# Kernel tuning notes

Measured on AMD Instinct MI355X. Metric: run time of the kernel, lower is better.

Reference implementation:

```python
import jax, jax.numpy as jnp
import numpy as np

NUM_GRAPHS = 1024
HIDDEN = 256
N_NODES = 500000


def setup_inputs() -> dict:
    key = jax.random.key(0)
    k1, k2, k3, k4 = jax.random.split(key, 4)
    x = jax.random.normal(k1, (N_NODES, HIDDEN), dtype=jnp.float32)
    batch = jnp.sort(jax.random.randint(k2, (N_NODES,), 0, NUM_GRAPHS, dtype=jnp.int64))
    # attention = nn.Linear(hidden_dim, 1): weight [1, hidden], bias [1]
    bound = 1.0 / np.sqrt(HIDDEN)
    att_w = jax.random.uniform(k3, (HIDDEN, 1), dtype=jnp.float32, minval=-bound, maxval=bound)
    att_b = jax.random.uniform(k4, (1,), dtype=jnp.float32, minval=-bound, maxval=bound)
    return {"x": x, "batch": batch, "att_w": att_w, "att_b": att_b}


def reference(x, batch, att_w, att_b):
    seg = batch.astype(jnp.int32)
    # mean pool: segment sum / counts
    sums = jax.ops.segment_sum(x, seg, num_segments=NUM_GRAPHS)  # [G, H]
    counts = jax.ops.segment_sum(jnp.ones((x.shape[0],), x.dtype), seg, num_segments=NUM_GRAPHS)
    mean_pool = sums / jnp.maximum(counts, 1.0)[:, None]
    # max pool
    max_pool = jax.ops.segment_max(x, seg, num_segments=NUM_GRAPHS)
    # attention-weighted add pool: sigmoid(x @ w + b) * x, segment-summed
    weights = jax.nn.sigmoid(x @ att_w + att_b)  # [N, 1]
    att_pool = jax.ops.segment_sum(x * weights, seg, num_segments=NUM_GRAPHS)
    return jnp.concatenate([mean_pool, max_pool, att_pool], axis=-1)
```

## Files before the change

kernel.cpp:

```cpp
#include <hip/hip_runtime.h>
#include <math.h>

constexpr int NUM_GRAPHS = 1024;

__global__ void detect_i32_kernel(const int* __restrict__ words, int n,
                                  int* __restrict__ flag) {
    const int stride = gridDim.x * blockDim.x;
    int acc = 0;
    for (int j = 1 + 2 * (int)(blockIdx.x * blockDim.x + threadIdx.x); j < n;
         j += 2 * stride)
        acc |= words[j];
    if (__any(acc != 0)) {
        if ((threadIdx.x & 63) == 0) atomicOr(flag, 1);
    }
}

__global__ void seg_start_kernel(const int* __restrict__ words, int n,
                                 const int* __restrict__ flag,
                                 int* __restrict__ seg) {
    int i = blockIdx.x * blockDim.x + threadIdx.x;
    if (i >= n) return;
    const bool is32 = (*flag != 0);
    int b    = is32 ? words[i] : words[2 * i];
    int prev = (i == 0) ? -1 : (is32 ? words[i - 1] : words[2 * (i - 1)]);
    for (int g = prev + 1; g <= b; ++g) seg[g] = i;
    if (i == n - 1)
        for (int g = b + 1; g <= NUM_GRAPHS; ++g) seg[g] = n;
}

__global__ __launch_bounds__(256) void pool_kernel(
    const float* __restrict__ x, const float* __restrict__ att_w,
    const float* __restrict__ att_b, const int* __restrict__ seg,
    float* __restrict__ out) {
    const int g    = blockIdx.x;
    const int lane = threadIdx.x & 63;
    const int w    = threadIdx.x >> 6;

    const int s0 = seg[g];
    const int e0 = seg[g + 1];

    const float4* __restrict__ x4 = (const float4*)x;
    const float4 wv   = ((const float4*)att_w)[lane];
    const float  bias = att_b[0];

    float sx = 0.f, sy = 0.f, sz = 0.f, sw = 0.f;
    float mx = -INFINITY, my = -INFINITY, mz = -INFINITY, mw = -INFINITY;
    float ax = 0.f, ay = 0.f, az = 0.f, aw = 0.f;

    auto proc4 = [&](const float4* v) {
        float p[4];
#pragma unroll
        for (int r = 0; r < 4; ++r)
            p[r] = v[r].x * wv.x + v[r].y * wv.y + v[r].z * wv.z + v[r].w * wv.w;
#pragma unroll
        for (int off = 32; off >= 1; off >>= 1) {
#pragma unroll
            for (int r = 0; r < 4; ++r)
                p[r] += __shfl_xor(p[r], off, 64);
        }
#pragma unroll
        for (int r = 0; r < 4; ++r) {
            const float sig = 1.0f / (1.0f + __expf(-(p[r] + bias)));
            sx += v[r].x; sy += v[r].y; sz += v[r].z; sw += v[r].w;
            mx = fmaxf(mx, v[r].x); my = fmaxf(my, v[r].y);
            mz = fmaxf(mz, v[r].z); mw = fmaxf(mw, v[r].w);
            ax += v[r].x * sig; ay += v[r].y * sig;
            az += v[r].z * sig; aw += v[r].w * sig;
        }
    };

    int i = s0 + w;
    if (i + 12 < e0) {
        float4 v[4];
#pragma unroll
        for (int r = 0; r < 4; ++r)
            v[r] = x4[(size_t)(i + 4 * r) * 64 + lane];
        int nb = i + 16;
        while (nb + 12 < e0) {
            float4 vn[4];
#pragma unroll
            for (int r = 0; r < 4; ++r)
                vn[r] = x4[(size_t)(nb + 4 * r) * 64 + lane];
            proc4(v);
#pragma unroll
            for (int r = 0; r < 4; ++r) v[r] = vn[r];
            nb += 16;
        }
        proc4(v);
        i = nb;
    }
    for (; i < e0; i += 4) {
        const float4 v = x4[(size_t)i * 64 + lane];
        float p = v.x * wv.x + v.y * wv.y + v.z * wv.z + v.w * wv.w;
#pragma unroll
        for (int off = 32; off >= 1; off >>= 1)
            p += __shfl_xor(p, off, 64);
        const float sig = 1.0f / (1.0f + __expf(-(p + bias)));
        sx += v.x; sy += v.y; sz += v.z; sw += v.w;
        mx = fmaxf(mx, v.x); my = fmaxf(my, v.y);
        mz = fmaxf(mz, v.z); mw = fmaxf(mw, v.w);
        ax += v.x * sig; ay += v.y * sig; az += v.z * sig; aw += v.w * sig;
    }

    __shared__ float4 lsum[4][64];
    __shared__ float4 lmax[4][64];
    __shared__ float4 latt[4][64];
    lsum[w][lane] = make_float4(sx, sy, sz, sw);
    lmax[w][lane] = make_float4(mx, my, mz, mw);
    latt[w][lane] = make_float4(ax, ay, az, aw);
    __syncthreads();

    if (w == 0) {
        float4 S = lsum[0][lane], M = lmax[0][lane], A = latt[0][lane];
#pragma unroll
        for (int ww = 1; ww < 4; ++ww) {
            float4 s2 = lsum[ww][lane], m2 = lmax[ww][lane], a2 = latt[ww][lane];
            S.x += s2.x; S.y += s2.y; S.z += s2.z; S.w += s2.w;
            M.x = fmaxf(M.x, m2.x); M.y = fmaxf(M.y, m2.y);
            M.z = fmaxf(M.z, m2.z); M.w = fmaxf(M.w, m2.w);
            A.x += a2.x; A.y += a2.y; A.z += a2.z; A.w += a2.w;
        }
        const int cnt = e0 - s0;
        const float inv = 1.0f / (float)(cnt > 0 ? cnt : 1);
        float4* __restrict__ o = (float4*)(out + (size_t)g * 768);
        o[lane]       = make_float4(S.x * inv, S.y * inv, S.z * inv, S.w * inv);
        o[64 + lane]  = M;
        o[128 + lane] = A;
    }
}

extern "C" void kernel_launch(void* const* d_in, const int* in_sizes, int n_in,
                              void* d_out, int out_size, void* d_ws, size_t ws_size,
                              hipStream_t stream) {
    const float* x           = (const float*)d_in[0];
    const int*   batch_words = (const int*)d_in[1];
    const float* att_w       = (const float*)d_in[2];
    const float* att_b       = (const float*)d_in[3];
    float*       out         = (float*)d_out;
    const int n = in_sizes[1];

    int* flag = (int*)d_ws;
    int* seg  = ((int*)d_ws) + 8;

    hipMemsetAsync(flag, 0, sizeof(int), stream);
    detect_i32_kernel<<<256, 256, 0, stream>>>(batch_words, n, flag);
    seg_start_kernel<<<(n + 255) / 256, 256, 0, stream>>>(batch_words, n, flag, seg);
    pool_kernel<<<NUM_GRAPHS, 256, 0, stream>>>(x, att_w, att_b, seg, out);
}
```

Before: 676.8 us.

## Split each graph's pooling across four blocks with a separate combine kernel

Each graph segment is now processed by four blocks instead of one, with rows interleaved across 16 waves. Each block writes its partial sum, max and attention-sum to workspace, and a second kernel combines the four partials and applies the mean division. This raises the block count from 1024 to 4096 to better fill the GPU's compute units and memory pipes while streaming the ~512MB input. The cost is an extra kernel launch plus partial-buffer traffic, and each block now gets fewer rows for its software-pipelined loop.

```diff
diff --git a/kernel.cpp b/kernel.cpp
--- a/kernel.cpp
+++ b/kernel.cpp
@@ -2,6 +2,9 @@
 #include <math.h>
 
 constexpr int NUM_GRAPHS = 1024;
+constexpr int QUARTERS   = 4;
+constexpr int WAVES_PB   = 4;
+constexpr int STRIDE     = QUARTERS * WAVES_PB;
 
 __global__ void detect_i32_kernel(const int* __restrict__ words, int n,
                                   int* __restrict__ flag) {
@@ -28,13 +31,15 @@
         for (int g = b + 1; g <= NUM_GRAPHS; ++g) seg[g] = n;
 }
 
-__global__ __launch_bounds__(256) void pool_kernel(
+__global__ __launch_bounds__(256) void pool_partial_kernel(
     const float* __restrict__ x, const float* __restrict__ att_w,
     const float* __restrict__ att_b, const int* __restrict__ seg,
-    float* __restrict__ out) {
-    const int g    = blockIdx.x;
+    float* __restrict__ part) {
+    const int g    = blockIdx.x >> 2;
+    const int q    = blockIdx.x & 3;
     const int lane = threadIdx.x & 63;
     const int w    = threadIdx.x >> 6;
+    const int W    = q * WAVES_PB + w;
 
     const int s0 = seg[g];
     const int e0 = seg[g + 1];
@@ -69,27 +74,27 @@
         }
     };
 
-    int i = s0 + w;
-    if (i + 12 < e0) {
+    int i = s0 + W;
+    if (i + 3 * STRIDE < e0) {
         float4 v[4];
 #pragma unroll
         for (int r = 0; r < 4; ++r)
-            v[r] = x4[(size_t)(i + 4 * r) * 64 + lane];
-        int nb = i + 16;
-        while (nb + 12 < e0) {
+            v[r] = x4[(size_t)(i + r * STRIDE) * 64 + lane];
+        int nb = i + 4 * STRIDE;
+        while (nb + 3 * STRIDE < e0) {
             float4 vn[4];
 #pragma unroll
             for (int r = 0; r < 4; ++r)
-                vn[r] = x4[(size_t)(nb + 4 * r) * 64 + lane];
+                vn[r] = x4[(size_t)(nb + r * STRIDE) * 64 + lane];
             proc4(v);
 #pragma unroll
             for (int r = 0; r < 4; ++r) v[r] = vn[r];
-            nb += 16;
+            nb += 4 * STRIDE;
         }
         proc4(v);
         i = nb;
     }
-    for (; i < e0; i += 4) {
+    for (; i < e0; i += STRIDE) {
         const float4 v = x4[(size_t)i * 64 + lane];
         float p = v.x * wv.x + v.y * wv.y + v.z * wv.z + v.w * wv.w;
 #pragma unroll
@@ -120,13 +125,46 @@
             M.z = fmaxf(M.z, m2.z); M.w = fmaxf(M.w, m2.w);
             A.x += a2.x; A.y += a2.y; A.z += a2.z; A.w += a2.w;
         }
-        const int cnt = e0 - s0;
-        const float inv = 1.0f / (float)(cnt > 0 ? cnt : 1);
-        float4* __restrict__ o = (float4*)(out + (size_t)g * 768);
-        o[lane]       = make_float4(S.x * inv, S.y * inv, S.z * inv, S.w * inv);
+        float4* __restrict__ o = (float4*)part + (size_t)blockIdx.x * 192;
+        o[lane]       = S;
         o[64 + lane]  = M;
         o[128 + lane] = A;
     }
+}
+
+__global__ __launch_bounds__(256) void pool_combine_kernel(
+    const float* __restrict__ part, const int* __restrict__ seg,
+    float* __restrict__ out) {
+    const int g = blockIdx.x;
+    const int t = threadIdx.x;
+    if (t >= 192) return;
+    const int sec  = t >> 6;
+    const int lane = t & 63;
+
+    const float4* __restrict__ p4 = (const float4*)part;
+    const size_t base = (size_t)g * 4 * 192 + sec * 64 + lane;
+
+    float4 a = p4[base];
+    if (sec == 1) {
+#pragma unroll
+        for (int q = 1; q < 4; ++q) {
+            float4 b = p4[base + (size_t)q * 192];
+            a.x = fmaxf(a.x, b.x); a.y = fmaxf(a.y, b.y);
+            a.z = fmaxf(a.z, b.z); a.w = fmaxf(a.w, b.w);
+        }
+    } else {
+#pragma unroll
+        for (int q = 1; q < 4; ++q) {
+            float4 b = p4[base + (size_t)q * 192];
+            a.x += b.x; a.y += b.y; a.z += b.z; a.w += b.w;
+        }
+        if (sec == 0) {
+            const int cnt = seg[g + 1] - seg[g];
+            const float inv = 1.0f / (float)(cnt > 0 ? cnt : 1);
+            a.x *= inv; a.y *= inv; a.z *= inv; a.w *= inv;
+        }
+    }
+    ((float4*)(out + (size_t)g * 768))[sec * 64 + lane] = a;
 }
 
 extern "C" void kernel_launch(void* const* d_in, const int* in_sizes, int n_in,
@@ -139,11 +177,13 @@
     float*       out         = (float*)d_out;
     const int n = in_sizes[1];
 
-    int* flag = (int*)d_ws;
-    int* seg  = ((int*)d_ws) + 8;
+    int*   flag = (int*)d_ws;
+    int*   seg  = ((int*)d_ws) + 8;
+    float* part = (float*)((char*)d_ws + 8192);
 
     hipMemsetAsync(flag, 0, sizeof(int), stream);
     detect_i32_kernel<<<256, 256, 0, stream>>>(batch_words, n, flag);
     seg_start_kernel<<<(n + 255) / 256, 256, 0, stream>>>(batch_words, n, flag, seg);
-    pool_kernel<<<NUM_GRAPHS, 256, 0, stream>>>(x, att_w, att_b, seg, out);
+    pool_partial_kernel<<<NUM_GRAPHS * QUARTERS, 256, 0, stream>>>(x, att_w, att_b, seg, part);
+    pool_combine_kernel<<<NUM_GRAPHS, 256, 0, stream>>>(part, seg, out);
 }
```

New measurement: 650.9 us. 1.04x faster.
